# Kernel tuning notes

Hardware: AMD Instinct MI355X
Metric: run time of the kernel (lower is better)

## Reference

```python
import jax, jax.numpy as jnp
from jax import lax
import numpy as np

B = 4096
CUR_OBS = 256; HIST_C = 96; HIST_T = 25
FUT_FLAT = 256 * 10  # fut_ref_dim * fut_ref_seq_len
HID = 1024; PROJ = 512; HLAT = 64; FLAT = 64
CONV = HID // 4  # conv_hidden_dim
E = 16; TOPK = 4; NGROUP = 4; TOPKG = 2; ROUTE_SCALE = 1.0; NSHARED = 2; OUT = 23

silu = jax.nn.silu

def conv1d(x, w, b, stride):
    # x: [B, C_in, T], w: [C_out, C_in, K] (torch Conv1d layout), padding=1
    y = lax.conv_general_dilated(x, w, (stride,), [(1, 1)],
                                 dimension_numbers=('NCH', 'OIH', 'NCH'))
    return y + b[None, :, None]

def setup_inputs() -> dict:
    key = jax.random.key(0)
    ks = iter(jax.random.split(key, 64))
    def nrm(shape, s=0.02):
        return jax.random.normal(next(ks), shape, jnp.float32) * s
    d = {}
    d['cur_obs'] = jax.random.normal(next(ks), (B, CUR_OBS), jnp.float32)
    d['cur_hist_seq'] = jax.random.normal(next(ks), (B, HIST_T, HIST_C), jnp.float32)
    d['fut_ref'] = jax.random.normal(next(ks), (B, FUT_FLAT), jnp.float32)
    d['vae_noise'] = jax.random.normal(next(ks), (B, FLAT), jnp.float32)
    # history conv encoder
    d['conv1_w'] = nrm((CONV, HIST_C, 3));      d['conv1_b'] = nrm((CONV,))
    d['conv2_w'] = nrm((2 * CONV, CONV, 3));    d['conv2_b'] = nrm((2 * CONV,))
    d['conv3_w'] = nrm((4 * CONV, 2 * CONV, 3)); d['conv3_b'] = nrm((4 * CONV,))
    d['hlin1_w'] = nrm((4 * CONV, HID)); d['hlin1_b'] = nrm((HID,))
    d['hlin2_w'] = nrm((HID, HLAT));     d['hlin2_b'] = nrm((HLAT,))
    # fut-ref VAE encoder
    d['enc1_w'] = nrm((FUT_FLAT, HID)); d['enc1_b'] = nrm((HID,))
    d['enc2_w'] = nrm((HID, HID));      d['enc2_b'] = nrm((HID,))
    d['enc3_w'] = nrm((HID, 2 * FLAT)); d['enc3_b'] = nrm((2 * FLAT,))
    # input projection
    d['proj_w'] = nrm((CUR_OBS + HLAT + FLAT, PROJ)); d['proj_b'] = nrm((PROJ,))
    # router
    d['router_w'] = nrm((PROJ, E)); d['router_b'] = nrm((E,))
    # stacked fine experts (DeepseekV3MLP x E)
    d['Wg'] = nrm((E, PROJ, HID)); d['bg'] = nrm((E, HID))
    d['Wu'] = nrm((E, PROJ, HID)); d['bu'] = nrm((E, HID))
    d['Wd'] = nrm((E, HID, PROJ)); d['bd'] = nrm((E, PROJ))
    # shared experts (intermediate = HID * NSHARED)
    d['sh_g_w'] = nrm((PROJ, HID * NSHARED)); d['sh_g_b'] = nrm((HID * NSHARED,))
    d['sh_u_w'] = nrm((PROJ, HID * NSHARED)); d['sh_u_b'] = nrm((HID * NSHARED,))
    d['sh_d_w'] = nrm((HID * NSHARED, PROJ)); d['sh_d_b'] = nrm((PROJ,))
    # output mlp + head
    d['out1_w'] = nrm((PROJ, HID)); d['out1_b'] = nrm((HID,))
    d['out2_w'] = nrm((HID, HID));  d['out2_b'] = nrm((HID,))
    d['head_w'] = nrm((HID, OUT));  d['head_b'] = nrm((OUT,))
    return d


def reference(cur_obs, cur_hist_seq, fut_ref, vae_noise,
              conv1_w, conv1_b, conv2_w, conv2_b, conv3_w, conv3_b,
              hlin1_w, hlin1_b, hlin2_w, hlin2_b,
              enc1_w, enc1_b, enc2_w, enc2_b, enc3_w, enc3_b,
              proj_w, proj_b, router_w, router_b,
              Wg, bg, Wu, bu, Wd, bd,
              sh_g_w, sh_g_b, sh_u_w, sh_u_b, sh_d_w, sh_d_b,
              out1_w, out1_b, out2_w, out2_b, head_w, head_b):
    # ---- history conv encoder ----
    h = cur_hist_seq.transpose(0, 2, 1)                 # [B, C, T]
    h = silu(conv1d(h, conv1_w, conv1_b, 1))            # [B, 256, 25]
    h = silu(conv1d(h, conv2_w, conv2_b, 2))            # [B, 512, 13]
    h = silu(conv1d(h, conv3_w, conv3_b, 2))            # [B, 1024, 7]
    h = h.mean(-1)                                      # AdaptiveAvgPool1d(1)+Flatten
    hist_lat = silu(h @ hlin1_w + hlin1_b) @ hlin2_w + hlin2_b  # [B, 64]
    # ---- fut-ref VAE encoder + reparameterize ----
    e = silu(fut_ref @ enc1_w + enc1_b)
    e = silu(e @ enc2_w + enc2_b)
    mu, logvar = jnp.split(e @ enc3_w + enc3_b, 2, axis=-1)
    z = mu + jnp.exp(0.5 * logvar) * vae_noise          # [B, 64]
    # ---- projection ----
    x = jnp.concatenate([cur_obs, hist_lat, z], axis=-1) @ proj_w + proj_b  # [B, PROJ]
    # ---- DeepseekV3 top-k group router (router math in fp32) ----
    logits = x.astype(jnp.float32) @ router_w + router_b
    scores = jax.nn.sigmoid(logits)                     # [B, E]
    gs = scores.reshape(-1, NGROUP, E // NGROUP)
    group_scores = lax.top_k(gs, 2)[0].sum(-1)          # [B, NGROUP]
    gidx = lax.top_k(group_scores, TOPKG)[1]
    rows = jnp.arange(scores.shape[0])[:, None]
    gmask = jnp.zeros_like(group_scores).at[rows, gidx].set(1.0)
    smask = jnp.repeat(gmask, E // NGROUP, axis=1)      # [B, E]
    masked = jnp.where(smask > 0, scores, 0.0)
    tidx = lax.top_k(masked, TOPK)[1]                   # [B, TOPK]
    tw = jnp.take_along_axis(scores, tidx, axis=1)
    tw = tw / (tw.sum(-1, keepdims=True) + 1e-20) * ROUTE_SCALE
    # ---- MoE dispatch/combine: sparse combine weights, dense expert eval ----
    w = jnp.zeros((x.shape[0], E), jnp.float32).at[rows, tidx].add(tw)  # [B, E]
    g = jnp.einsum('bh,ehi->bei', x, Wg) + bg           # [B, E, HID]
    u = jnp.einsum('bh,ehi->bei', x, Wu) + bu
    y = jnp.einsum('bei,eih->beh', silu(g) * u, Wd) + bd  # [B, E, PROJ]
    moe_out = jnp.einsum('be,beh->bh', w, y)            # [B, PROJ]
    shared = (silu(x @ sh_g_w + sh_g_b) * (x @ sh_u_w + sh_u_b)) @ sh_d_w + sh_d_b
    h2 = moe_out + shared
    h2 = silu(h2 @ out1_w + out1_b) @ out2_w + out2_b
    return h2 @ head_w + head_b                         # actions [B, OUT]
```

## Files before the change

### kernel.cpp

```cpp
#include <hip/hip_runtime.h>
#include <hip/hip_bf16.h>


#define BATCH 4096
typedef unsigned short u16;
typedef unsigned int u32;
using bf16x8 = __attribute__((ext_vector_type(8))) __bf16;
using f32x4  = __attribute__((ext_vector_type(4))) float;

__device__ __forceinline__ float silu_f(float v) { return v / (1.f + __expf(-v)); }

__device__ __forceinline__ float b2f(u16 u) {
  union { u32 i; float f; } c; c.i = ((u32)u) << 16; return c.f;
}
__device__ __forceinline__ u16 f2b(float f) {
  union { float f; u32 i; } c; c.f = f;
  u32 r = c.i + 0x7FFFu + ((c.i >> 16) & 1u);
  return (u16)(r >> 16);
}
__device__ __forceinline__ float4 ld4(const float* p) { return *(const float4*)p; }
__device__ __forceinline__ float4 ld4(const u16* p) {
  ushort4 v = *(const ushort4*)p;
  return make_float4(b2f(v.x), b2f(v.y), b2f(v.z), b2f(v.w));
}

__device__ __forceinline__ void gll16(const u16* g, u16* l) {
  __attribute__((address_space(3))) u32* lp =
      reinterpret_cast<__attribute__((address_space(3))) u32*>(
          reinterpret_cast<uintptr_t>(l));
  __builtin_amdgcn_global_load_lds(reinterpret_cast<const u32*>(g), lp, 16, 0, 0);
}

union U8 { uint4 u; bf16x8 b; };

static constexpr size_t WT1T_B = 0;
static constexpr size_t WT2T_B = 147456;
static constexpr size_t WT3T_B = 933888;
static constexpr size_t HL1T_B = 4079616;
static constexpr size_t RA_B   = 6176768;
static constexpr size_t RB_B   = 64897024;
static constexpr size_t P_B    = 119422976;
static constexpr size_t FRH_B  = RA_B;
static constexpr size_t FRL_B  = RA_B + 20971520;
static constexpr size_t E1H_B  = RA_B + 41943040;
static constexpr size_t E1L_B  = RA_B + 50331648;
static constexpr size_t E2H_B  = RA_B;
static constexpr size_t E2L_B  = RA_B + 8388608;
static constexpr size_t Y1_B   = RA_B;
static constexpr size_t Y3_B   = RA_B;
static constexpr size_t WGT_B  = RA_B;
static constexpr size_t WUT_B  = RA_B + 16777216;
static constexpr size_t WDT_B  = RA_B + 33554432;
static constexpr size_t X_B    = RA_B + 50331648;
static constexpr size_t SHGT_B = RA_B;
static constexpr size_t SHUT_B = RA_B + 2097152;
static constexpr size_t SHDT_B = RA_B + 4194304;
static constexpr size_t O1T_B  = RA_B + 6291456;
static constexpr size_t O2T_B  = RA_B + 7340032;
static constexpr size_t H2_B   = RA_B + 25165824;
static constexpr size_t H2B_B  = RA_B + 33554432;
static constexpr size_t E1TH_B = RB_B;
static constexpr size_t E1TL_B = RB_B + 5242880;
static constexpr size_t E2TH_B = RB_B + 10485760;
static constexpr size_t E2TL_B = RB_B + 12582912;
static constexpr size_t PENC_B = RB_B + 14680064;
static constexpr size_t HSB_B  = RB_B;
static constexpr size_t Y2_B   = RB_B;
static constexpr size_t HB_B   = RB_B;
static constexpr size_t HI1_B  = RB_B + 8388608;
static constexpr size_t XCH_B  = RB_B + 16777216;
static constexpr size_t XCL_B  = RB_B + 19922944;
static constexpr size_t XH_B   = RB_B;
static constexpr size_t TM_B   = RB_B + 8388608;
static constexpr size_t STB_B  = RB_B + 8388608;
static constexpr size_t O1B_B  = RB_B;
static constexpr size_t O2H_B  = RB_B + 16777216;
static constexpr size_t O2L_B  = RB_B + 25165824;
static constexpr size_t HLAT_B = P_B;
static constexpr size_t E3P_B  = P_B + 1048576;
static constexpr size_t Z_B    = P_B + 3145728;
static constexpr size_t LOG_B  = P_B + 4194304;
static constexpr size_t TID_B  = P_B + 4456448;
static constexpr size_t TW_B   = P_B + 4521984;
static constexpr size_t POS_B  = P_B + 4587520;
static constexpr size_t CNT_B  = P_B + 4653056;
static constexpr size_t OFS_B  = P_B + 4653184;
static constexpr size_t ROWL_B = P_B + 4653312;
static constexpr size_t WL_B   = P_B + 4718848;
static constexpr size_t ZP_B   = P_B + 4784384;
static constexpr size_t PRJH_B = P_B + 4788480;
static constexpr size_t PRJL_B = P_B + 5181696;
static constexpr size_t E3TH_B = P_B + 5574912;
static constexpr size_t E3TL_B = P_B + 5837056;
static constexpr size_t HL2P_B = P_B + 6099200;
static constexpr size_t HDH_B  = P_B + 6361344;
static constexpr size_t HDL_B  = P_B + 6623488;

#define TILE_DECODE(nn_)                         \
  const int bid = blockIdx.x;                    \
  const int xcd = bid & 7;                       \
  const int tt_ = bid >> 3;                      \
  const int n0 = (tt_ % (nn_)) * 128;            \
  const int m0 = ((tt_ / (nn_)) * 8 + xcd) * 128;

__global__ void k_zero_i(int* __restrict__ p, int n) {
  int i = blockIdx.x * 64 + threadIdx.x;
  if (i < n) p[i] = 0;
}
__global__ void k_zero_f4(float4* __restrict__ p, int n4) {
  int i = blockIdx.x * 256 + threadIdx.x;
  if (i < n4) p[i] = make_float4(0.f, 0.f, 0.f, 0.f);
}
__global__ void k_f32_to_bf4(const float* __restrict__ s, u16* __restrict__ d, int n4) {
  int i = blockIdx.x * 256 + threadIdx.x;
  if (i >= n4) return;
  float4 v = *(const float4*)(s + (size_t)i * 4);
  *(ushort4*)(d + (size_t)i * 4) = make_ushort4(f2b(v.x), f2b(v.y), f2b(v.z), f2b(v.w));
}
__global__ void k_split_x(const float* __restrict__ s, u16* __restrict__ dh,
                          u16* __restrict__ dl, int n4) {
  int i = blockIdx.x * 256 + threadIdx.x;
  if (i >= n4) return;
  float4 v = *(const float4*)(s + (size_t)i * 4);
  float a[4] = {v.x, v.y, v.z, v.w};
  ushort4 h, l;
  u16* hp = (u16*)&h; u16* lp = (u16*)&l;
#pragma unroll
  for (int j = 0; j < 4; ++j) {
    u16 hh = f2b(a[j]);
    hp[j] = hh;
    lp[j] = f2b(a[j] - b2f(hh));
  }
  *(ushort4*)(dh + (size_t)i * 4) = h;
  *(ushort4*)(dl + (size_t)i * 4) = l;
}
template<int ACT>
__global__ void k_comb2(const float* __restrict__ P0, const float* __restrict__ P1,
                        const float* __restrict__ bias, u16* __restrict__ Ch,
                        u16* __restrict__ Cl, int N, int n4) {
  int i = blockIdx.x * 256 + threadIdx.x;
  if (i >= n4) return;
  float4 a = *(const float4*)(P0 + (size_t)i * 4);
  float4 b = *(const float4*)(P1 + (size_t)i * 4);
  int col = (i * 4) & (N - 1);
  float r[4] = {a.x + b.x, a.y + b.y, a.z + b.z, a.w + b.w};
  ushort4 h, l;
  u16* hp = (u16*)&h; u16* lp = (u16*)&l;
#pragma unroll
  for (int j = 0; j < 4; ++j) {
    float v = r[j] + bias[col + j];
    if (ACT) v = silu_f(v);
    u16 hh = f2b(v);
    hp[j] = hh;
    lp[j] = f2b(v - b2f(hh));
  }
  *(ushort4*)(Ch + (size_t)i * 4) = h;
  *(ushort4*)(Cl + (size_t)i * 4) = l;
}
__global__ void k_concat_split(const float* __restrict__ obs,
                               const float* __restrict__ hl,
                               const float* __restrict__ z,
                               u16* __restrict__ dh, u16* __restrict__ dl) {
  int idx = blockIdx.x * 256 + threadIdx.x;
  if (idx >= BATCH * 384) return;
  int b = idx / 384, c = idx - b * 384;
  float v;
  if (c < 256)      v = obs[(size_t)b * 256 + c];
  else if (c < 320) v = hl[(size_t)b * 64 + (c - 256)];
  else              v = z[(size_t)b * 64 + (c - 320)];
  u16 h = f2b(v);
  dh[idx] = h;
  dl[idx] = f2b(v - b2f(h));
}
__global__ void k_wt_conv(const float* __restrict__ w, u16* __restrict__ wt,
                          int CIN, int COUT) {
  int idx = blockIdx.x * 256 + threadIdx.x;
  int Kc = CIN * 3;
  if (idx >= COUT * Kc) return;
  int o = idx / Kc, c = idx - o * Kc;
  int k = c / CIN, i = c - k * CIN;
  wt[idx] = f2b(w[(size_t)o * Kc + i * 3 + k]);
}
__global__ __launch_bounds__(256) void k_transpose_bf(const float* __restrict__ W,
                                                      u16* __restrict__ WT,
                                                      int K, int N) {
  __shared__ float t[32][33];
  int n0 = blockIdx.x * 32, k0 = blockIdx.y * 32;
  int lx = threadIdx.x & 31, ly = threadIdx.x >> 5;
#pragma unroll
  for (int r = 0; r < 32; r += 8)
    t[ly + r][lx] = W[(size_t)(k0 + ly + r) * N + n0 + lx];
  __syncthreads();
#pragma unroll
  for (int r = 0; r < 32; r += 8)
    WT[(size_t)(n0 + ly + r) * K + k0 + lx] = f2b(t[lx][ly + r]);
}
__global__ __launch_bounds__(256) void k_transpose_bf_pad(const float* __restrict__ W,
                                                          u16* __restrict__ WT,
                                                          int K, int N) {
  __shared__ float t[32][33];
  int n0 = blockIdx.x * 32, k0 = blockIdx.y * 32;
  int lx = threadIdx.x & 31, ly = threadIdx.x >> 5;
#pragma unroll
  for (int r = 0; r < 32; r += 8)
    t[ly + r][lx] = (n0 + lx < N) ? W[(size_t)(k0 + ly + r) * N + n0 + lx] : 0.f;
  __syncthreads();
#pragma unroll
  for (int r = 0; r < 32; r += 8)
    WT[(size_t)(n0 + ly + r) * K + k0 + lx] = f2b(t[lx][ly + r]);
}
__global__ __launch_bounds__(256) void k_transpose_hilo_pad(const float* __restrict__ W,
                                                            u16* __restrict__ WTh,
                                                            u16* __restrict__ WTl,
                                                            int K, int N) {
  __shared__ float t[32][33];
  int n0 = blockIdx.x * 32, k0 = blockIdx.y * 32;
  int lx = threadIdx.x & 31, ly = threadIdx.x >> 5;
#pragma unroll
  for (int r = 0; r < 32; r += 8)
    t[ly + r][lx] = (n0 + lx < N) ? W[(size_t)(k0 + ly + r) * N + n0 + lx] : 0.f;
  __syncthreads();
#pragma unroll
  for (int r = 0; r < 32; r += 8) {
    float f = t[lx][ly + r];
    u16 h = f2b(f);
    size_t o = (size_t)(n0 + ly + r) * K + k0 + lx;
    WTh[o] = h;
    WTl[o] = f2b(f - b2f(h));
  }
}
__global__ __launch_bounds__(256) void k_transpose_bf_b(const float* __restrict__ W,
                                                        u16* __restrict__ WT,
                                                        int K, int N) {
  const size_t eo = (size_t)blockIdx.z * K * N;
  __shared__ float t[32][33];
  int n0 = blockIdx.x * 32, k0 = blockIdx.y * 32;
  int lx = threadIdx.x & 31, ly = threadIdx.x >> 5;
#pragma unroll
  for (int r = 0; r < 32; r += 8)
    t[ly + r][lx] = W[eo + (size_t)(k0 + ly + r) * N + n0 + lx];
  __syncthreads();
#pragma unroll
  for (int r = 0; r < 32; r += 8)
    WT[eo + (size_t)(n0 + ly + r) * K + k0 + lx] = f2b(t[lx][ly + r]);
}
__global__ __launch_bounds__(256) void k_transpose_hilo(const float* __restrict__ W,
                                                        u16* __restrict__ WTh,
                                                        u16* __restrict__ WTl,
                                                        int K, int N) {
  __shared__ float t[32][33];
  int n0 = blockIdx.x * 32, k0 = blockIdx.y * 32;
  int lx = threadIdx.x & 31, ly = threadIdx.x >> 5;
#pragma unroll
  for (int r = 0; r < 32; r += 8)
    t[ly + r][lx] = W[(size_t)(k0 + ly + r) * N + n0 + lx];
  __syncthreads();
#pragma unroll
  for (int r = 0; r < 32; r += 8) {
    float f = t[lx][ly + r];
    u16 h = f2b(f);
    size_t o = (size_t)(n0 + ly + r) * K + k0 + lx;
    WTh[o] = h;
    WTl[o] = f2b(f - b2f(h));
  }
// ... 24 lines not shown
  const u16* sA0 = A0 + (size_t)(m0 + r0) * lda + sl;
  const u16* sA1 = (AP == 2) ? A1 + (size_t)(m0 + r0) * lda + sl : nullptr;
  const u16* sB0 = B0 + (size_t)(n0 + r0) * ldb + sl;
  const u16* sB1 = (BP == 2) ? B1 + (size_t)(n0 + r0) * ldb + sl : nullptr;
  const size_t stepA = (size_t)16 * lda, stepB = (size_t)16 * ldb;
  const int wb = wid * 1024;

  f32x4 acc[4][4];
  const f32x4 zf = {0.f, 0.f, 0.f, 0.f};
#pragma unroll
  for (int i = 0; i < 4; ++i)
#pragma unroll
    for (int j = 0; j < 4; ++j) acc[i][j] = zf;

  for (int k0 = 0; k0 < K; k0 += 32) {
    {
      int t = 0;
      gll16(sA0 + k0, &lds[t * 4096 + wb]);
      gll16(sA0 + stepA + k0, &lds[t * 4096 + wb + 512]);
      ++t;
      if (AP == 2) {
        gll16(sA1 + k0, &lds[t * 4096 + wb]);
        gll16(sA1 + stepA + k0, &lds[t * 4096 + wb + 512]);
        ++t;
      }
      gll16(sB0 + k0, &lds[t * 4096 + wb]);
      gll16(sB0 + stepB + k0, &lds[t * 4096 + wb + 512]);
      ++t;
      if (BP == 2) {
        gll16(sB1 + k0, &lds[t * 4096 + wb]);
        gll16(sB1 + stepB + k0, &lds[t * 4096 + wb + 512]);
      }
    }
    __syncthreads();
    U8 fah[4], fal[4];
#pragma unroll
    for (int i = 0; i < 4; ++i) {
      int ra = wr + i * 16 + l15;
      int ao = ra * 32 + ((lsub ^ ((ra >> 1) & 3))) * 8;
      fah[i].u = *(const uint4*)&lds[ao];
      if (AP == 2) fal[i].u = *(const uint4*)&lds[4096 + ao];
    }
#pragma unroll
    for (int ni = 0; ni < 4; ++ni) {
      int rb = wc + ni * 16 + l15;
      int bo = AP * 4096 + rb * 32 + ((lsub ^ ((rb >> 1) & 3))) * 8;
      U8 fbh, fbl;
      fbh.u = *(const uint4*)&lds[bo];
      if (BP == 2) fbl.u = *(const uint4*)&lds[4096 + bo];
#pragma unroll
      for (int mi = 0; mi < 4; ++mi) {
        acc[mi][ni] = MFMA_BF16(fah[mi].b, fbh.b, acc[mi][ni]);
        if (BP == 2) acc[mi][ni] = MFMA_BF16(fah[mi].b, fbl.b, acc[mi][ni]);
        if (AP == 2) acc[mi][ni] = MFMA_BF16(fal[mi].b, fbh.b, acc[mi][ni]);
      }
    }
    __syncthreads();
  }
  const int row4 = lsub * 4;
#pragma unroll
  for (int mi = 0; mi < 4; ++mi)
#pragma unroll
    for (int ni = 0; ni < 4; ++ni) {
      int col = n0 + wc + ni * 16 + l15;
      if (col >= Nout) continue;
      float bv = bias[col];
#pragma unroll
      for (int j = 0; j < 4; ++j) {
        int row = m0 + wr + mi * 16 + row4 + j;
        float v = acc[mi][ni][j] + bv;
        if (ACT) v = silu_f(v);
        if (EPI == 0) Cf[(size_t)row * Nout + col] = v;
        else if (EPI == 1) Ch[(size_t)row * Nout + col] = f2b(v);
        else if (EPI == 2) Cf[(size_t)row * Nout + col] += v;
        else {
          u16 vh = f2b(v);
          Ch[(size_t)row * Nout + col] = vh;
          Cl[(size_t)row * Nout + col] = f2b(v - b2f(vh));
        }
      }
    }
}

template<int ACT, int EPI>
__global__ __launch_bounds__(256) void k_gg64(
    const u16* __restrict__ A0, const u16* __restrict__ B0,
    const float* __restrict__ bias,
    float* __restrict__ Cf, u16* __restrict__ Ch, u16* __restrict__ Cl,
    int K, int lda, int ldb, int nn, int Nout) {
  __shared__ u16 lds[2 * 8192];
  PRO128
  TILE_DECODE(nn)
  const int soff = ((lane & 7) ^ (lane >> 3)) * 8;
  const u16* sAb = A0 + (size_t)(m0 + wid * 32 + (lane >> 3)) * lda + soff;
  const u16* sBb = B0 + (size_t)(n0 + wid * 32 + (lane >> 3)) * ldb + soff;
  const int wb = wid * 2048;

  f32x4 acc[4][4];
  const f32x4 zf = {0.f, 0.f, 0.f, 0.f};
#pragma unroll
  for (int i = 0; i < 4; ++i)
#pragma unroll
    for (int j = 0; j < 4; ++j) acc[i][j] = zf;

  for (int k0 = 0; k0 < K; k0 += 64) {
#pragma unroll
    for (int c = 0; c < 4; ++c) {
      gll16(sAb + (size_t)c * 8 * lda + k0, &lds[wb + c * 512]);
      gll16(sBb + (size_t)c * 8 * ldb + k0, &lds[8192 + wb + c * 512]);
    }
    __syncthreads();
#pragma unroll
    for (int h = 0; h < 2; ++h) {
      U8 fa[4], fb[4];
#pragma unroll
      for (int i = 0; i < 4; ++i) {
        int ra = wr + i * 16 + l15;
        fa[i].u = *(const uint4*)&lds[ra * 64 + (((h * 4 + lsub) ^ (ra & 7))) * 8];
        int rb = wc + i * 16 + l15;
        fb[i].u = *(const uint4*)&lds[8192 + rb * 64 + (((h * 4 + lsub) ^ (rb & 7))) * 8];
      }
#pragma unroll
      for (int mi = 0; mi < 4; ++mi)
#pragma unroll
        for (int ni = 0; ni < 4; ++ni)
          acc[mi][ni] = MFMA_BF16(fa[mi].b, fb[ni].b, acc[mi][ni]);
    }
    __syncthreads();
  }
  const int row4 = lsub * 4;
#pragma unroll
  for (int mi = 0; mi < 4; ++mi)
#pragma unroll
    for (int ni = 0; ni < 4; ++ni) {
      int col = n0 + wc + ni * 16 + l15;
      if (col >= Nout) continue;
      float bv = bias[col];
#pragma unroll
      for (int j = 0; j < 4; ++j) {
        int row = m0 + wr + mi * 16 + row4 + j;
        float v = acc[mi][ni][j] + bv;
        if (ACT) v = silu_f(v);
        if (EPI == 0) Cf[(size_t)row * Nout + col] = v;
        else if (EPI == 1) Ch[(size_t)row * Nout + col] = f2b(v);
        else if (EPI == 2) Cf[(size_t)row * Nout + col] += v;
        else {
          u16 vh = f2b(v);
          Ch[(size_t)row * Nout + col] = vh;
          Cl[(size_t)row * Nout + col] = f2b(v - b2f(vh));
        }
      }
    }
}

__global__ __launch_bounds__(256) void k_ggp(
    const u16* __restrict__ A0, const u16* __restrict__ A1,
    const u16* __restrict__ B0, const u16* __restrict__ B1,
    float* __restrict__ P, int N, int Kh, int lda, int ldb, int nn) {
  __shared__ u16 lds[4 * 4096];
  PRO128
  const int bid = blockIdx.x;
  const int xcd = bid & 7;
  int t = bid >> 3;
  const int kh = t & 1; t >>= 1;
  const int n0 = (t % nn) * 128;
  const int m0 = ((t / nn) * 8 + xcd) * 128;
  const int koff = kh * Kh;
  const int r0 = wid * 32 + (lane >> 2);
  const int sl = ((lane & 3) ^ ((r0 >> 1) & 3)) * 8;
  const u16* sA0 = A0 + (size_t)(m0 + r0) * lda + sl + koff;
  const u16* sA1 = A1 + (size_t)(m0 + r0) * lda + sl + koff;
  const u16* sB0 = B0 + (size_t)(n0 + r0) * ldb + sl + koff;
  const u16* sB1 = B1 + (size_t)(n0 + r0) * ldb + sl + koff;
  const size_t stepA = (size_t)16 * lda, stepB = (size_t)16 * ldb;
  const int wb = wid * 1024;

  f32x4 acc[4][4];
  const f32x4 zf = {0.f, 0.f, 0.f, 0.f};
#pragma unroll
  for (int i = 0; i < 4; ++i)
#pragma unroll
    for (int j = 0; j < 4; ++j) acc[i][j] = zf;

  for (int k0 = 0; k0 < Kh; k0 += 32) {
    gll16(sA0 + k0, &lds[wb]);
    gll16(sA0 + stepA + k0, &lds[wb + 512]);
    gll16(sA1 + k0, &lds[4096 + wb]);
    gll16(sA1 + stepA + k0, &lds[4096 + wb + 512]);
    gll16(sB0 + k0, &lds[2 * 4096 + wb]);
    gll16(sB0 + stepB + k0, &lds[2 * 4096 + wb + 512]);
    gll16(sB1 + k0, &lds[3 * 4096 + wb]);
    gll16(sB1 + stepB + k0, &lds[3 * 4096 + wb + 512]);
    __syncthreads();
    U8 fah[4], fal[4];
#pragma unroll
    for (int i = 0; i < 4; ++i) {
      int ra = wr + i * 16 + l15;
      int ao = ra * 32 + ((lsub ^ ((ra >> 1) & 3))) * 8;
      fah[i].u = *(const uint4*)&lds[ao];
      fal[i].u = *(const uint4*)&lds[4096 + ao];
    }
#pragma unroll
    for (int ni = 0; ni < 4; ++ni) {
      int rb = wc + ni * 16 + l15;
      int bo = 2 * 4096 + rb * 32 + ((lsub ^ ((rb >> 1) & 3))) * 8;
      U8 fbh, fbl;
      fbh.u = *(const uint4*)&lds[bo];
      fbl.u = *(const uint4*)&lds[4096 + bo];
#pragma unroll
      for (int mi = 0; mi < 4; ++mi) {
        acc[mi][ni] = MFMA_BF16(fah[mi].b, fbh.b, acc[mi][ni]);
        acc[mi][ni] = MFMA_BF16(fah[mi].b, fbl.b, acc[mi][ni]);
        acc[mi][ni] = MFMA_BF16(fal[mi].b, fbh.b, acc[mi][ni]);
      }
    }
    __syncthreads();
  }
  float* Pk = P + (size_t)kh * ((size_t)BATCH * N);
  const int row4 = lsub * 4;
#pragma unroll
  for (int mi = 0; mi < 4; ++mi)
#pragma unroll
    for (int ni = 0; ni < 4; ++ni) {
      int col = n0 + wc + ni * 16 + l15;
#pragma unroll
      for (int j = 0; j < 4; ++j) {
        int row = m0 + wr + mi * 16 + row4 + j;
        Pk[(size_t)row * N + col] = acc[mi][ni][j];
      }
    }
}

__global__ __launch_bounds__(256) void k_gdual1(
    const u16* __restrict__ A0, const u16* __restrict__ G0,
    const u16* __restrict__ U0,
    const float* __restrict__ bg, const float* __restrict__ bu,
    u16* __restrict__ C, int N, int K, int lda, int ldb, int nn) {
  __shared__ u16 lds[3 * 4096];
  PRO128
  TILE_DECODE(nn)
  const int r0 = wid * 32 + (lane >> 2);
  const int sl = ((lane & 3) ^ ((r0 >> 1) & 3)) * 8;
  const u16* sA = A0 + (size_t)(m0 + r0) * lda + sl;
  const u16* sG = G0 + (size_t)(n0 + r0) * ldb + sl;
  const u16* sU = U0 + (size_t)(n0 + r0) * ldb + sl;
  const size_t stepA = (size_t)16 * lda, stepB = (size_t)16 * ldb;
  const int wb = wid * 1024;
  f32x4 ag[4][4], au[4][4];
  const f32x4 zf = {0.f, 0.f, 0.f, 0.f};
#pragma unroll
  for (int i = 0; i < 4; ++i)
#pragma unroll
    for (int j = 0; j < 4; ++j) { ag[i][j] = zf; au[i][j] = zf; }

  for (int k0 = 0; k0 < K; k0 += 32) {
    gll16(sA + k0, &lds[wb]);
    gll16(sA + stepA + k0, &lds[wb + 512]);
    gll16(sG + k0, &lds[4096 + wb]);
    gll16(sG + stepB + k0, &lds[4096 + wb + 512]);
    gll16(sU + k0, &lds[2 * 4096 + wb]);
    gll16(sU + stepB + k0, &lds[2 * 4096 + wb + 512]);
    __syncthreads();
    U8 fa[4];
#pragma unroll
    for (int i = 0; i < 4; ++i) {
      int ra = wr + i * 16 + l15;
      fa[i].u = *(const uint4*)&lds[ra * 32 + ((lsub ^ ((ra >> 1) & 3))) * 8];
    }
#pragma unroll
    for (int ni = 0; ni < 4; ++ni) {
      int rb = wc + ni * 16 + l15;
      int bo = rb * 32 + ((lsub ^ ((rb >> 1) & 3))) * 8;
      U8 fg, fu;
      fg.u = *(const uint4*)&lds[4096 + bo];
      fu.u = *(const uint4*)&lds[2 * 4096 + bo];
#pragma unroll
      for (int mi = 0; mi < 4; ++mi) {
        ag[mi][ni] = MFMA_BF16(fa[mi].b, fg.b, ag[mi][ni]);
        au[mi][ni] = MFMA_BF16(fa[mi].b, fu.b, au[mi][ni]);
      }
    }
    __syncthreads();
  }
  const int row4 = lsub * 4;
#pragma unroll
  for (int mi = 0; mi < 4; ++mi)
#pragma unroll
    for (int ni = 0; ni < 4; ++ni) {
      int col = n0 + wc + ni * 16 + l15;
      float bgv = bg[col], buv = bu[col];
#pragma unroll
      for (int j = 0; j < 4; ++j) {
        int row = m0 + wr + mi * 16 + row4 + j;
        float v = silu_f(ag[mi][ni][j] + bgv) * (au[mi][ni][j] + buv);
        C[(size_t)row * N + col] = f2b(v);
      }
    }
}

template<int CIN, int TIN, int TOUT, int STRIDE>
__global__ __launch_bounds__(256) void k_gconv32(
    const u16* __restrict__ X, const u16* __restrict__ WT,
    const float* __restrict__ bias, u16* __restrict__ Y,
    const u16* __restrict__ zp, int COUT, int nn) {
  constexpr int K = CIN * 3;
  __shared__ u16 lds[2 * 4096];
  PRO128
  TILE_DECODE(nn)
  int bA_[2], tb_[2], sl_[2];
  const u16* sB[2];
#pragma unroll
// ... 442 lines not shown
  int e = tidA[idx];
  int p = offs[e] + posA[idx];
  rowlist[p] = idx >> 2;
  wlist[p] = twA[idx];
}

extern "C" void kernel_launch(void* const* d_in, const int* in_sizes, int n_in,
                              void* d_out, int out_size, void* d_ws, size_t ws_size,
                              hipStream_t stream) {
  const float* cur_obs  = (const float*)d_in[0];
  const float* hist_seq = (const float*)d_in[1];
  const float* fut_ref  = (const float*)d_in[2];
  const float* noise    = (const float*)d_in[3];
  const float* conv1_w  = (const float*)d_in[4];
  const float* conv1_b  = (const float*)d_in[5];
  const float* conv2_w  = (const float*)d_in[6];
  const float* conv2_b  = (const float*)d_in[7];
  const float* conv3_w  = (const float*)d_in[8];
  const float* conv3_b  = (const float*)d_in[9];
  const float* hlin1_w  = (const float*)d_in[10];
  const float* hlin1_b  = (const float*)d_in[11];
  const float* hlin2_w  = (const float*)d_in[12];
  const float* hlin2_b  = (const float*)d_in[13];
  const float* enc1_w   = (const float*)d_in[14];
  const float* enc1_b   = (const float*)d_in[15];
  const float* enc2_w   = (const float*)d_in[16];
  const float* enc2_b   = (const float*)d_in[17];
  const float* enc3_w   = (const float*)d_in[18];
  const float* enc3_b   = (const float*)d_in[19];
  const float* proj_w   = (const float*)d_in[20];
  const float* proj_b   = (const float*)d_in[21];
  const float* router_w = (const float*)d_in[22];
  const float* router_b = (const float*)d_in[23];
  const float* Wg       = (const float*)d_in[24];
  const float* bg       = (const float*)d_in[25];
  const float* Wu       = (const float*)d_in[26];
  const float* bu       = (const float*)d_in[27];
  const float* Wd       = (const float*)d_in[28];
  const float* bd       = (const float*)d_in[29];
  const float* shg_w    = (const float*)d_in[30];
  const float* shg_b    = (const float*)d_in[31];
  const float* shu_w    = (const float*)d_in[32];
  const float* shu_b    = (const float*)d_in[33];
  const float* shd_w    = (const float*)d_in[34];
  const float* shd_b    = (const float*)d_in[35];
  const float* out1_w   = (const float*)d_in[36];
  const float* out1_b   = (const float*)d_in[37];
  const float* out2_w   = (const float*)d_in[38];
  const float* out2_b   = (const float*)d_in[39];
  const float* head_w   = (const float*)d_in[40];
  const float* head_b   = (const float*)d_in[41];
  (void)in_sizes; (void)n_in; (void)out_size; (void)ws_size;

  char* wsb = (char*)d_ws;
  u16* wt1T  = (u16*)(wsb + WT1T_B);
  u16* wt2T  = (u16*)(wsb + WT2T_B);
  u16* wt3T  = (u16*)(wsb + WT3T_B);
  u16* hl1T  = (u16*)(wsb + HL1T_B);
  u16* frh   = (u16*)(wsb + FRH_B);
  u16* frl   = (u16*)(wsb + FRL_B);
  u16* e1h   = (u16*)(wsb + E1H_B);
  u16* e1l   = (u16*)(wsb + E1L_B);
  u16* e2h   = (u16*)(wsb + E2H_B);
  u16* e2l   = (u16*)(wsb + E2L_B);
  u16* y1b   = (u16*)(wsb + Y1_B);
  u16* y2b   = (u16*)(wsb + Y2_B);
  u16* y3b   = (u16*)(wsb + Y3_B);
  u16* wgT   = (u16*)(wsb + WGT_B);
  u16* wuT   = (u16*)(wsb + WUT_B);
  u16* wdT   = (u16*)(wsb + WDT_B);
  float* x   = (float*)(wsb + X_B);
  u16* shgT  = (u16*)(wsb + SHGT_B);
  u16* shuT  = (u16*)(wsb + SHUT_B);
  u16* shdT  = (u16*)(wsb + SHDT_B);
  u16* o1T   = (u16*)(wsb + O1T_B);
  u16* o2T   = (u16*)(wsb + O2T_B);
  float* h2  = (float*)(wsb + H2_B);
  u16* h2b   = (u16*)(wsb + H2B_B);
  u16* e1Th  = (u16*)(wsb + E1TH_B);
  u16* e1Tl  = (u16*)(wsb + E1TL_B);
  u16* e2Th  = (u16*)(wsb + E2TH_B);
  u16* e2Tl  = (u16*)(wsb + E2TL_B);
  float* Penc = (float*)(wsb + PENC_B);
  u16* hsb   = (u16*)(wsb + HSB_B);
  u16* hb    = (u16*)(wsb + HB_B);
  u16* hi1b  = (u16*)(wsb + HI1_B);
  u16* xch   = (u16*)(wsb + XCH_B);
  u16* xcl   = (u16*)(wsb + XCL_B);
  u16* xh    = (u16*)(wsb + XH_B);
  u16* tmoeb = (u16*)(wsb + TM_B);
  u16* stb   = (u16*)(wsb + STB_B);
  u16* o1b   = (u16*)(wsb + O1B_B);
  u16* o2h   = (u16*)(wsb + O2H_B);
  u16* o2l   = (u16*)(wsb + O2L_B);
  float* hlat = (float*)(wsb + HLAT_B);
  float* e3   = (float*)(wsb + E3P_B);
  float* z    = (float*)(wsb + Z_B);
  float* logitsb = (float*)(wsb + LOG_B);
  int*   tidA  = (int*)(wsb + TID_B);
  float* twA   = (float*)(wsb + TW_B);
  int*   posA  = (int*)(wsb + POS_B);
  int*   counts = (int*)(wsb + CNT_B);
  int*   offs  = (int*)(wsb + OFS_B);
  int*   rowlist = (int*)(wsb + ROWL_B);
  float* wlist = (float*)(wsb + WL_B);
  u16*   zp    = (u16*)(wsb + ZP_B);
  u16* prjTh = (u16*)(wsb + PRJH_B);
  u16* prjTl = (u16*)(wsb + PRJL_B);
  u16* e3Th  = (u16*)(wsb + E3TH_B);
  u16* e3Tl  = (u16*)(wsb + E3TL_B);
  u16* hl2P  = (u16*)(wsb + HL2P_B);
  u16* hdTh  = (u16*)(wsb + HDH_B);
  u16* hdTl  = (u16*)(wsb + HDL_B);

  k_zero_i<<<dim3(1), 64, 0, stream>>>(counts, 16);
  k_zero_i<<<dim3(16), 64, 0, stream>>>((int*)zp, 1024);

  k_wt_conv<<<dim3(288), 256, 0, stream>>>(conv1_w, wt1T, 96, 256);
  k_wt_conv<<<dim3(1536), 256, 0, stream>>>(conv2_w, wt2T, 256, 512);
  k_wt_conv<<<dim3(6144), 256, 0, stream>>>(conv3_w, wt3T, 512, 1024);
  k_transpose_bf<<<dim3(32, 32), 256, 0, stream>>>(hlin1_w, hl1T, 1024, 1024);
  k_transpose_hilo<<<dim3(32, 80), 256, 0, stream>>>(enc1_w, e1Th, e1Tl, 2560, 1024);
  k_transpose_hilo<<<dim3(32, 32), 256, 0, stream>>>(enc2_w, e2Th, e2Tl, 1024, 1024);
  k_transpose_hilo<<<dim3(4, 32), 256, 0, stream>>>(enc3_w, e3Th, e3Tl, 1024, 128);
  k_transpose_hilo<<<dim3(16, 12), 256, 0, stream>>>(proj_w, prjTh, prjTl, 384, 512);
  k_transpose_bf_pad<<<dim3(4, 32), 256, 0, stream>>>(hlin2_w, hl2P, 1024, 64);
  k_transpose_hilo_pad<<<dim3(4, 32), 256, 0, stream>>>(head_w, hdTh, hdTl, 1024, 23);

  k_split_x<<<dim3(10240), 256, 0, stream>>>(fut_ref, frh, frl, BATCH * 2560 / 4);
  k_ggp<<<dim3(512), 256, 0, stream>>>(frh, frl, e1Th, e1Tl, Penc,
                                       1024, 1280, 2560, 2560, 8);
  k_comb2<1><<<dim3(4096), 256, 0, stream>>>(Penc, Penc + (size_t)BATCH * 1024,
                                             enc1_b, e1h, e1l, 1024, BATCH * 1024 / 4);
  k_ggp<<<dim3(512), 256, 0, stream>>>(e1h, e1l, e2Th, e2Tl, Penc,
                                       1024, 512, 1024, 1024, 8);
  k_comb2<1><<<dim3(4096), 256, 0, stream>>>(Penc, Penc + (size_t)BATCH * 1024,
                                             enc2_b, e2h, e2l, 1024, BATCH * 1024 / 4);
  k_gg<0, 0, 2, 2><<<dim3(32), 256, 0, stream>>>(e2h, e2l, e3Th, e3Tl, enc3_b,
      e3, nullptr, nullptr, 1024, 1024, 1024, 1, 128);
  k_z<<<dim3(1024), 256, 0, stream>>>(e3, noise, z);

  k_f32_to_bf4<<<dim3(9600), 256, 0, stream>>>(hist_seq, hsb, BATCH * 25 * 96 / 4);
  k_gconv32<96, 25, 25, 1><<<dim3(1600), 256, 0, stream>>>(hsb, wt1T, conv1_b, y1b, zp, 256, 2);
  k_gconv64<256, 25, 13, 2><<<dim3(1664), 256, 0, stream>>>(y1b, wt2T, conv2_b, y2b, zp, 512, 4);
  k_gconv64<512, 13, 7, 2><<<dim3(1792), 256, 0, stream>>>(y2b, wt3T, conv3_b, y3b, zp, 1024, 8);
  k_mean7<<<dim3(16384), 256, 0, stream>>>(y3b, hb);
  k_gg64<1, 1><<<dim3(256), 256, 0, stream>>>(hb, hl1T, hlin1_b,
      nullptr, hi1b, nullptr, 1024, 1024, 1024, 8, 1024);
  k_gg64<0, 0><<<dim3(32), 256, 0, stream>>>(hi1b, hl2P, hlin2_b,
      hlat, nullptr, nullptr, 1024, 1024, 1024, 1, 64);

  k_transpose_bf_b<<<dim3(32, 16, 16), 256, 0, stream>>>(Wg, wgT, 512, 1024);
  k_transpose_bf_b<<<dim3(32, 16, 16), 256, 0, stream>>>(Wu, wuT, 512, 1024);
  k_transpose_bf_b<<<dim3(16, 32, 16), 256, 0, stream>>>(Wd, wdT, 1024, 512);

  k_concat_split<<<dim3(6144), 256, 0, stream>>>(cur_obs, hlat, z, xch, xcl);
  k_gg<0, 0, 2, 2><<<dim3(128), 256, 0, stream>>>(xch, xcl, prjTh, prjTl, proj_b,
      x, nullptr, nullptr, 384, 384, 384, 4, 512);
  k_gemm<0, true, float><<<dim3(64, 1), 256, 0, stream>>>(x, router_w, router_b, logitsb, 16, 512);
  k_router<<<dim3(16), 256, 0, stream>>>(logitsb, tidA, twA, posA, counts);
  k_offsets<<<dim3(1), 64, 0, stream>>>(counts, offs);
  k_build<<<dim3(64), 256, 0, stream>>>(tidA, twA, posA, offs, rowlist, wlist);
  k_f32_to_bf4<<<dim3(2048), 256, 0, stream>>>(x, xh, BATCH * 512 / 4);

  k_gmoeup<<<dim3(4096), 256, 0, stream>>>(xh, wgT, wuT, bg, bu,
                                           rowlist, counts, offs, zp, tmoeb);

  k_transpose_bf<<<dim3(64, 16), 256, 0, stream>>>(shg_w, shgT, 512, 2048);
  k_transpose_bf<<<dim3(64, 16), 256, 0, stream>>>(shu_w, shuT, 512, 2048);
  k_transpose_bf<<<dim3(16, 64), 256, 0, stream>>>(shd_w, shdT, 2048, 512);
  k_transpose_bf<<<dim3(32, 16), 256, 0, stream>>>(out1_w, o1T, 512, 1024);
  k_transpose_bf<<<dim3(32, 32), 256, 0, stream>>>(out2_w, o2T, 1024, 1024);
  k_zero_f4<<<dim3(2048), 256, 0, stream>>>((float4*)h2, BATCH * 512 / 4);

  k_gmoedown64<<<dim3(2048), 256, 0, stream>>>(tmoeb, wdT, bd, rowlist, wlist,
                                               counts, offs, zp, h2);

  k_gdual1<<<dim3(512), 256, 0, stream>>>(xh, shgT, shuT, shg_b, shu_b,
                                          stb, 2048, 512, 512, 512, 16);
  k_gg64<0, 2><<<dim3(128), 256, 0, stream>>>(stb, shdT, shd_b,
      h2, nullptr, nullptr, 2048, 2048, 2048, 4, 512);

  k_f32_to_bf4<<<dim3(2048), 256, 0, stream>>>(h2, h2b, BATCH * 512 / 4);
  k_gg64<1, 1><<<dim3(256), 256, 0, stream>>>(h2b, o1T, out1_b,
      nullptr, o1b, nullptr, 512, 512, 512, 8, 1024);
  k_gg64<0, 3><<<dim3(256), 256, 0, stream>>>(o1b, o2T, out2_b,
      nullptr, o2h, o2l, 1024, 1024, 1024, 8, 1024);
  k_gg<0, 0, 2, 2><<<dim3(32), 256, 0, stream>>>(o2h, o2l, hdTh, hdTl, head_b,
      (float*)d_out, nullptr, nullptr, 1024, 1024, 1024, 1, 23);
}
```

Baseline: 1.060 ms.

## Use split-K GEMMs for narrow low-occupancy layers and fuse small prep launches

Generalizes the two-way split-K GEMM into a kernel with a configurable split count and hi/lo precision options. It applies it to the narrow GEMMs (enc3, hlin2, head, shared-down), which previously launched only 32 or 128 blocks, and adds a reduction kernel that sums the partials, adds bias and writes or accumulates the output. It also merges the zeroing launches and the three conv weight transposes into single kernels. The aim is to fill more CUs on the skinny GEMMs, at the cost of extra partial-sum traffic through global memory and an additional reduction launch per layer.

```diff
diff --git a/kernel.cpp b/kernel.cpp
--- a/kernel.cpp
+++ b/kernel.cpp
@@ -68,14 +68,17 @@
 static constexpr size_t Y2_B   = RB_B;
 static constexpr size_t HB_B   = RB_B;
 static constexpr size_t HI1_B  = RB_B + 8388608;
+static constexpr size_t PHL2_B = RB_B + 16777216;
 static constexpr size_t XCH_B  = RB_B + 16777216;
 static constexpr size_t XCL_B  = RB_B + 19922944;
 static constexpr size_t XH_B   = RB_B;
 static constexpr size_t TM_B   = RB_B + 8388608;
 static constexpr size_t STB_B  = RB_B + 8388608;
+static constexpr size_t PSH_B  = RB_B + 25165824;
 static constexpr size_t O1B_B  = RB_B;
 static constexpr size_t O2H_B  = RB_B + 16777216;
 static constexpr size_t O2L_B  = RB_B + 25165824;
+static constexpr size_t PHD_B  = RB_B + 33554432;
 static constexpr size_t HLAT_B = P_B;
 static constexpr size_t E3P_B  = P_B + 1048576;
 static constexpr size_t Z_B    = P_B + 3145728;
@@ -103,9 +106,10 @@
   const int n0 = (tt_ % (nn_)) * 128;            \
   const int m0 = ((tt_ / (nn_)) * 8 + xcd) * 128;
 
-__global__ void k_zero_i(int* __restrict__ p, int n) {
-  int i = blockIdx.x * 64 + threadIdx.x;
-  if (i < n) p[i] = 0;
+__global__ void k_zero2(int* __restrict__ a, int na, int* __restrict__ b, int nb) {
+  int i = blockIdx.x * 256 + threadIdx.x;
+  if (i < na) a[i] = 0;
+  else if (i < na + nb) b[i - na] = 0;
 }
 __global__ void k_zero_f4(float4* __restrict__ p, int n4) {
   int i = blockIdx.x * 256 + threadIdx.x;
@@ -156,6 +160,21 @@
   }
   *(ushort4*)(Ch + (size_t)i * 4) = h;
   *(ushort4*)(Cl + (size_t)i * 4) = l;
+}
+template<int ACT, int EPI>
+__global__ void k_combS(const float* __restrict__ P, const float* __restrict__ bias,
+                        float* __restrict__ Cf, int S, int lgNp, int Nout, int total) {
+  int idx = blockIdx.x * 256 + threadIdx.x;
+  if (idx >= total) return;
+  int row = idx >> lgNp;
+  int col = idx & ((1 << lgNp) - 1);
+  if (col >= Nout) return;
+  float s = 0.f;
+  for (int si = 0; si < S; ++si) s += P[(size_t)si * total + idx];
+  s += bias[col];
+  if (ACT) s = silu_f(s);
+  if (EPI == 0) Cf[(size_t)row * Nout + col] = s;
+  else Cf[(size_t)row * Nout + col] += s;
 }
 __global__ void k_concat_split(const float* __restrict__ obs,
                                const float* __restrict__ hl,
@@ -172,14 +191,19 @@
   dh[idx] = h;
   dl[idx] = f2b(v - b2f(h));
 }
-__global__ void k_wt_conv(const float* __restrict__ w, u16* __restrict__ wt,
-                          int CIN, int COUT) {
+__global__ void k_wt_conv3(const float* __restrict__ w1, u16* __restrict__ t1,
+                           const float* __restrict__ w2, u16* __restrict__ t2,
+                           const float* __restrict__ w3, u16* __restrict__ t3) {
   int idx = blockIdx.x * 256 + threadIdx.x;
+  const float* w; u16* t; int CIN;
+  if (idx < 73728)        { w = w1; t = t1; CIN = 96; }
+  else if (idx < 466944)  { idx -= 73728;  w = w2; t = t2; CIN = 256; }
+  else if (idx < 2039808) { idx -= 466944; w = w3; t = t3; CIN = 512; }
+  else return;
   int Kc = CIN * 3;
-  if (idx >= COUT * Kc) return;
   int o = idx / Kc, c = idx - o * Kc;
   int k = c / CIN, i = c - k * CIN;
-  wt[idx] = f2b(w[(size_t)o * Kc + i * 3 + k]);
+  t[idx] = f2b(w[(size_t)o * Kc + i * 3 + k]);
 }
 __global__ __launch_bounds__(256) void k_transpose_bf(const float* __restrict__ W,
                                                       u16* __restrict__ WT,
@@ -370,6 +394,97 @@
     }
 }
 
+template<int AP, int BP>
+__global__ __launch_bounds__(256) void k_ggps(
+    const u16* __restrict__ A0, const u16* __restrict__ A1,
+    const u16* __restrict__ B0, const u16* __restrict__ B1,
+    float* __restrict__ P, int Kh, int lda, int ldb, int nn, int Nt, int base) {
+  constexpr int NT = AP + BP;
+  __shared__ u16 lds[NT * 4096];
+  PRO128
+  const int bidx = blockIdx.x;
+  const int kh = bidx / base;
+  const int b2 = bidx - kh * base;
+  const int xcd = b2 & 7;
+  const int tt_ = b2 >> 3;
+  const int n0 = (tt_ % nn) * 128;
+  const int m0 = ((tt_ / nn) * 8 + xcd) * 128;
+  const int koff = kh * Kh;
+  const int r0 = wid * 32 + (lane >> 2);
+  const int sl = ((lane & 3) ^ ((r0 >> 1) & 3)) * 8;
+  const u16* sA0 = A0 + (size_t)(m0 + r0) * lda + sl + koff;
+  const u16* sA1 = (AP == 2) ? A1 + (size_t)(m0 + r0) * lda + sl + koff : nullptr;
+  const u16* sB0 = B0 + (size_t)(n0 + r0) * ldb + sl + koff;
+  const u16* sB1 = (BP == 2) ? B1 + (size_t)(n0 + r0) * ldb + sl + koff : nullptr;
+  const size_t stepA = (size_t)16 * lda, stepB = (size_t)16 * ldb;
+  const int wb = wid * 1024;
+
+  f32x4 acc[4][4];
+  const f32x4 zf = {0.f, 0.f, 0.f, 0.f};
+#pragma unroll
+  for (int i = 0; i < 4; ++i)
+#pragma unroll
+    for (int j = 0; j < 4; ++j) acc[i][j] = zf;
+
+  for (int k0 = 0; k0 < Kh; k0 += 32) {
+    {
+      int t = 0;
+      gll16(sA0 + k0, &lds[t * 4096 + wb]);
+      gll16(sA0 + stepA + k0, &lds[t * 4096 + wb + 512]);
+      ++t;
+      if (AP == 2) {
+        gll16(sA1 + k0, &lds[t * 4096 + wb]);
+        gll16(sA1 + stepA + k0, &lds[t * 4096 + wb + 512]);
+        ++t;
+      }
+      gll16(sB0 + k0, &lds[t * 4096 + wb]);
+      gll16(sB0 + stepB + k0, &lds[t * 4096 + wb + 512]);
+      ++t;
+      if (BP == 2) {
+        gll16(sB1 + k0, &lds[t * 4096 + wb]);
+        gll16(sB1 + stepB + k0, &lds[t * 4096 + wb + 512]);
+      }
+    }
+    __syncthreads();
+    U8 fah[4], fal[4];
+#pragma unroll
+    for (int i = 0; i < 4; ++i) {
+      int ra = wr + i * 16 + l15;
+      int ao = ra * 32 + ((lsub ^ ((ra >> 1) & 3))) * 8;
+      fah[i].u = *(const uint4*)&lds[ao];
+      if (AP == 2) fal[i].u = *(const uint4*)&lds[4096 + ao];
+    }
+#pragma unroll
+    for (int ni = 0; ni < 4; ++ni) {
+      int rb = wc + ni * 16 + l15;
+      int bo = AP * 4096 + rb * 32 + ((lsub ^ ((rb >> 1) & 3))) * 8;
+      U8 fbh, fbl;
+      fbh.u = *(const uint4*)&lds[bo];
+      if (BP == 2) fbl.u = *(const uint4*)&lds[4096 + bo];
+#pragma unroll
+      for (int mi = 0; mi < 4; ++mi) {
+        acc[mi][ni] = MFMA_BF16(fah[mi].b, fbh.b, acc[mi][ni]);
+        if (BP == 2) acc[mi][ni] = MFMA_BF16(fah[mi].b, fbl.b, acc[mi][ni]);
+        if (AP == 2) acc[mi][ni] = MFMA_BF16(fal[mi].b, fbh.b, acc[mi][ni]);
+      }
+    }
+    __syncthreads();
+  }
+  float* Pk = P + (size_t)kh * ((size_t)BATCH * Nt);
+  const int row4 = lsub * 4;
+#pragma unroll
+  for (int mi = 0; mi < 4; ++mi)
+#pragma unroll
+    for (int ni = 0; ni < 4; ++ni) {
+      int col = n0 + wc + ni * 16 + l15;
+#pragma unroll
+      for (int j = 0; j < 4; ++j) {
+        int row = m0 + wr + mi * 16 + row4 + j;
+        Pk[(size_t)row * Nt + col] = acc[mi][ni][j];
+      }
+    }
+}
+
 template<int ACT, int EPI>
 __global__ __launch_bounds__(256) void k_gg64(
     const u16* __restrict__ A0, const u16* __restrict__ B0,
@@ -437,84 +552,6 @@
           Ch[(size_t)row * Nout + col] = vh;
           Cl[(size_t)row * Nout + col] = f2b(v - b2f(vh));
         }
-      }
-    }
-}
-
-__global__ __launch_bounds__(256) void k_ggp(
-    const u16* __restrict__ A0, const u16* __restrict__ A1,
-    const u16* __restrict__ B0, const u16* __restrict__ B1,
-    float* __restrict__ P, int N, int Kh, int lda, int ldb, int nn) {
-  __shared__ u16 lds[4 * 4096];
-  PRO128
-  const int bid = blockIdx.x;
-  const int xcd = bid & 7;
-  int t = bid >> 3;
-  const int kh = t & 1; t >>= 1;
-  const int n0 = (t % nn) * 128;
-  const int m0 = ((t / nn) * 8 + xcd) * 128;
-  const int koff = kh * Kh;
-  const int r0 = wid * 32 + (lane >> 2);
-  const int sl = ((lane & 3) ^ ((r0 >> 1) & 3)) * 8;
-  const u16* sA0 = A0 + (size_t)(m0 + r0) * lda + sl + koff;
-  const u16* sA1 = A1 + (size_t)(m0 + r0) * lda + sl + koff;
-  const u16* sB0 = B0 + (size_t)(n0 + r0) * ldb + sl + koff;
-  const u16* sB1 = B1 + (size_t)(n0 + r0) * ldb + sl + koff;
-  const size_t stepA = (size_t)16 * lda, stepB = (size_t)16 * ldb;
-  const int wb = wid * 1024;
-
-  f32x4 acc[4][4];
-  const f32x4 zf = {0.f, 0.f, 0.f, 0.f};
-#pragma unroll
-  for (int i = 0; i < 4; ++i)
-#pragma unroll
-    for (int j = 0; j < 4; ++j) acc[i][j] = zf;
-
-  for (int k0 = 0; k0 < Kh; k0 += 32) {
-    gll16(sA0 + k0, &lds[wb]);
-    gll16(sA0 + stepA + k0, &lds[wb + 512]);
-    gll16(sA1 + k0, &lds[4096 + wb]);
-    gll16(sA1 + stepA + k0, &lds[4096 + wb + 512]);
-    gll16(sB0 + k0, &lds[2 * 4096 + wb]);
-    gll16(sB0 + stepB + k0, &lds[2 * 4096 + wb + 512]);
-    gll16(sB1 + k0, &lds[3 * 4096 + wb]);
-    gll16(sB1 + stepB + k0, &lds[3 * 4096 + wb + 512]);
-    __syncthreads();
-    U8 fah[4], fal[4];
-#pragma unroll
-    for (int i = 0; i < 4; ++i) {
-      int ra = wr + i * 16 + l15;
-      int ao = ra * 32 + ((lsub ^ ((ra >> 1) & 3))) * 8;
-      fah[i].u = *(const uint4*)&lds[ao];
-      fal[i].u = *(const uint4*)&lds[4096 + ao];
-    }
-#pragma unroll
-    for (int ni = 0; ni < 4; ++ni) {
-      int rb = wc + ni * 16 + l15;
-      int bo = 2 * 4096 + rb * 32 + ((lsub ^ ((rb >> 1) & 3))) * 8;
-      U8 fbh, fbl;
-      fbh.u = *(const uint4*)&lds[bo];
-      fbl.u = *(const uint4*)&lds[4096 + bo];
-#pragma unroll
-      for (int mi = 0; mi < 4; ++mi) {
-        acc[mi][ni] = MFMA_BF16(fah[mi].b, fbh.b, acc[mi][ni]);
-        acc[mi][ni] = MFMA_BF16(fah[mi].b, fbl.b, acc[mi][ni]);
-        acc[mi][ni] = MFMA_BF16(fal[mi].b, fbh.b, acc[mi][ni]);
-      }
-    }
-    __syncthreads();
-  }
-  float* Pk = P + (size_t)kh * ((size_t)BATCH * N);
-  const int row4 = lsub * 4;
-#pragma unroll
-  for (int mi = 0; mi < 4; ++mi)
-#pragma unroll
-    for (int ni = 0; ni < 4; ++ni) {
-      int col = n0 + wc + ni * 16 + l15;
-#pragma unroll
-      for (int j = 0; j < 4; ++j) {
-        int row = m0 + wr + mi * 16 + row4 + j;
-        Pk[(size_t)row * N + col] = acc[mi][ni][j];
       }
     }
 }
@@ -1123,6 +1160,9 @@
   u16* e2Th  = (u16*)(wsb + E2TH_B);
   u16* e2Tl  = (u16*)(wsb + E2TL_B);
   float* Penc = (float*)(wsb + PENC_B);
+  float* Phl2 = (float*)(wsb + PHL2_B);
+  float* Psh  = (float*)(wsb + PSH_B);
+  float* Phd  = (float*)(wsb + PHD_B);
   u16* hsb   = (u16*)(wsb + HSB_B);
   u16* hb    = (u16*)(wsb + HB_B);
   u16* hi1b  = (u16*)(wsb + HI1_B);
@@ -1154,12 +1194,9 @@
   u16* hdTh  = (u16*)(wsb + HDH_B);
   u16* hdTl  = (u16*)(wsb + HDL_B);
 
-  k_zero_i<<<dim3(1), 64, 0, stream>>>(counts, 16);
-  k_zero_i<<<dim3(16), 64, 0, stream>>>((int*)zp, 1024);
-
-  k_wt_conv<<<dim3(288), 256, 0, stream>>>(conv1_w, wt1T, 96, 256);
-  k_wt_conv<<<dim3(1536), 256, 0, stream>>>(conv2_w, wt2T, 256, 512);
-  k_wt_conv<<<dim3(6144), 256, 0, stream>>>(conv3_w, wt3T, 512, 1024);
+  k_zero2<<<dim3(5), 256, 0, stream>>>(counts, 16, (int*)zp, 1024);
+
+  k_wt_conv3<<<dim3(7968), 256, 0, stream>>>(conv1_w, wt1T, conv2_w, wt2T, conv3_w, wt3T);
   k_transpose_bf<<<dim3(32, 32), 256, 0, stream>>>(hlin1_w, hl1T, 1024, 1024);
   k_transpose_hilo<<<dim3(32, 80), 256, 0, stream>>>(enc1_w, e1Th, e1Tl, 2560, 1024);
   k_transpose_hilo<<<dim3(32, 32), 256, 0, stream>>>(enc2_w, e2Th, e2Tl, 1024, 1024);
@@ -1169,16 +1206,17 @@
   k_transpose_hilo_pad<<<dim3(4, 32), 256, 0, stream>>>(head_w, hdTh, hdTl, 1024, 23);
 
   k_split_x<<<dim3(10240), 256, 0, stream>>>(fut_ref, frh, frl, BATCH * 2560 / 4);
-  k_ggp<<<dim3(512), 256, 0, stream>>>(frh, frl, e1Th, e1Tl, Penc,
-                                       1024, 1280, 2560, 2560, 8);
+  k_ggps<2, 2><<<dim3(512), 256, 0, stream>>>(frh, frl, e1Th, e1Tl, Penc,
+                                              1280, 2560, 2560, 8, 1024, 256);
   k_comb2<1><<<dim3(4096), 256, 0, stream>>>(Penc, Penc + (size_t)BATCH * 1024,
                                              enc1_b, e1h, e1l, 1024, BATCH * 1024 / 4);
-  k_ggp<<<dim3(512), 256, 0, stream>>>(e1h, e1l, e2Th, e2Tl, Penc,
-                                       1024, 512, 1024, 1024, 8);
+  k_ggps<2, 2><<<dim3(512), 256, 0, stream>>>(e1h, e1l, e2Th, e2Tl, Penc,
+                                              512, 1024, 1024, 8, 1024, 256);
   k_comb2<1><<<dim3(4096), 256, 0, stream>>>(Penc, Penc + (size_t)BATCH * 1024,
                                              enc2_b, e2h, e2l, 1024, BATCH * 1024 / 4);
-  k_gg<0, 0, 2, 2><<<dim3(32), 256, 0, stream>>>(e2h, e2l, e3Th, e3Tl, enc3_b,
-      e3, nullptr, nullptr, 1024, 1024, 1024, 1, 128);
+  k_ggps<2, 2><<<dim3(128), 256, 0, stream>>>(e2h, e2l, e3Th, e3Tl, Penc,
+                                              256, 1024, 1024, 1, 128, 32);
+  k_combS<0, 0><<<dim3(2048), 256, 0, stream>>>(Penc, enc3_b, e3, 4, 7, 128, BATCH * 128);
   k_z<<<dim3(1024), 256, 0, stream>>>(e3, noise, z);
 
   k_f32_to_bf4<<<dim3(9600), 256, 0, stream>>>(hist_seq, hsb, BATCH * 25 * 96 / 4);
@@ -1188,8 +1226,9 @@
   k_mean7<<<dim3(16384), 256, 0, stream>>>(y3b, hb);
   k_gg64<1, 1><<<dim3(256), 256, 0, stream>>>(hb, hl1T, hlin1_b,
       nullptr, hi1b, nullptr, 1024, 1024, 1024, 8, 1024);
-  k_gg64<0, 0><<<dim3(32), 256, 0, stream>>>(hi1b, hl2P, hlin2_b,
-      hlat, nullptr, nullptr, 1024, 1024, 1024, 1, 64);
+  k_ggps<1, 1><<<dim3(128), 256, 0, stream>>>(hi1b, nullptr, hl2P, nullptr, Phl2,
+                                              256, 1024, 1024, 1, 128, 32);
+  k_combS<0, 0><<<dim3(2048), 256, 0, stream>>>(Phl2, hlin2_b, hlat, 4, 7, 64, BATCH * 128);
 
   k_transpose_bf_b<<<dim3(32, 16, 16), 256, 0, stream>>>(Wg, wgT, 512, 1024);
   k_transpose_bf_b<<<dim3(32, 16, 16), 256, 0, stream>>>(Wu, wuT, 512, 1024);
@@ -1219,14 +1258,16 @@
 
   k_gdual1<<<dim3(512), 256, 0, stream>>>(xh, shgT, shuT, shg_b, shu_b,
                                           stb, 2048, 512, 512, 512, 16);
-  k_gg64<0, 2><<<dim3(128), 256, 0, stream>>>(stb, shdT, shd_b,
-      h2, nullptr, nullptr, 2048, 2048, 2048, 4, 512);
+  k_ggps<1, 1><<<dim3(256), 256, 0, stream>>>(stb, nullptr, shdT, nullptr, Psh,
+                                              1024, 2048, 2048, 4, 512, 128);
+  k_combS<0, 2><<<dim3(8192), 256, 0, stream>>>(Psh, shd_b, h2, 2, 9, 512, BATCH * 512);
 
   k_f32_to_bf4<<<dim3(2048), 256, 0, stream>>>(h2, h2b, BATCH * 512 / 4);
   k_gg64<1, 1><<<dim3(256), 256, 0, stream>>>(h2b, o1T, out1_b,
       nullptr, o1b, nullptr, 512, 512, 512, 8, 1024);
   k_gg64<0, 3><<<dim3(256), 256, 0, stream>>>(o1b, o2T, out2_b,
       nullptr, o2h, o2l, 1024, 1024, 1024, 8, 1024);
-  k_gg<0, 0, 2, 2><<<dim3(32), 256, 0, stream>>>(o2h, o2l, hdTh, hdTl, head_b,
-      (float*)d_out, nullptr, nullptr, 1024, 1024, 1024, 1, 23);
-}
+  k_ggps<2, 2><<<dim3(128), 256, 0, stream>>>(o2h, o2l, hdTh, hdTl, Phd,
+                                              256, 1024, 1024, 1, 128, 32);
+  k_combS<0, 0><<<dim3(2048), 256, 0, stream>>>(Phd, head_b, (float*)d_out, 4, 7, 23, BATCH * 128);
+}
```

New measurement: 991.4 us. 6.5% less time.
